# Optimization experiments

Measured on AMD Instinct MI355X. Metric: run time of the kernel, lower is better.

## Reference

```python
import jax, jax.numpy as jnp
import numpy as np

N = 20000      # nodes
E = 640000     # edges (avg degree 32)
F = 6          # feature_dim
D = 128        # weight_dim
L = 3          # lstm num_layers
DEPTH = 10     # extra iterations after initial call


def setup_inputs() -> dict:
    key = jax.random.key(0)
    ks = jax.random.split(key, 10)
    s = 0.05
    return {
        "features": jax.random.normal(ks[0], (N, F), jnp.float32),
        "src": jax.random.randint(ks[1], (E,), 0, N),
        "dst": jax.random.randint(ks[2], (E,), 0, N),
        "W_in": jax.random.normal(ks[3], (F, D), jnp.float32) * s,
        "b_in": jnp.zeros((D,), jnp.float32),
        "Wih0": jax.random.normal(ks[4], (4 * D, 2 * D), jnp.float32) * s,   # layer 0: input = concat(h_in, feat)
        "Wih_rest": jax.random.normal(ks[5], (2, 4 * D, D), jnp.float32) * s,  # layers 1,2
        "Whh": jax.random.normal(ks[6], (L, 4 * D, D), jnp.float32) * s,
        "bih": jnp.zeros((L, 4 * D), jnp.float32),
        "bhh": jnp.zeros((L, 4 * D), jnp.float32),
        "W_out": jax.random.normal(ks[7], (D, 1), jnp.float32) * s,
        "b_out": jnp.zeros((1,), jnp.float32),
    }


def _lstm_cell(x, h, c, Wih, Whh, b):
    # PyTorch gate order: i, f, g, o
    gates = x @ Wih.T + h @ Whh.T + b              # [N, 4D]
    i, f, g, o = jnp.split(gates, 4, axis=-1)
    i = jax.nn.sigmoid(i)
    f = jax.nn.sigmoid(f)
    o = jax.nn.sigmoid(o)
    g = jnp.tanh(g)
    c_new = f * c + i * g
    h_new = o * jnp.tanh(c_new)
    return h_new, c_new


def reference(features, src, dst, W_in, b_in, Wih0, Wih_rest, Whh, bih, bhh, W_out, b_out):
    n = features.shape[0]
    b = bih + bhh                                   # [L, 4D]

    def agg(x):
        # DGL update_all(copy_src, mean): mean over incoming edges (src -> dst)
        s = jax.ops.segment_sum(x[src], dst, num_segments=n)
        deg = jax.ops.segment_sum(jnp.ones((src.shape[0],), x.dtype), dst, num_segments=n)
        return jnp.where(deg[:, None] > 0, s / jnp.maximum(deg, 1.0)[:, None], 0.0)

    feat = jax.nn.relu(features @ W_in + b_in)      # [N, D]
    h = jnp.zeros((L, n, D), features.dtype)
    c = jnp.zeros((L, n, D), features.dtype)

    def step(carry, _):
        feat, h, c = carry
        x0 = jnp.concatenate([agg(feat), feat], axis=-1)   # [N, 2D]
        h0, c0 = _lstm_cell(x0, h[0], c[0], Wih0, Whh[0], b[0])
        h1, c1 = _lstm_cell(h0, h[1], c[1], Wih_rest[0], Whh[1], b[1])
        h2, c2 = _lstm_cell(h1, h[2], c[2], Wih_rest[1], Whh[2], b[2])
        return (h2, jnp.stack([h0, h1, h2]), jnp.stack([c0, c1, c2])), None

    # initial call + depth extra iterations, all structurally identical
    (feat, h, c), _ = jax.lax.scan(step, (feat, h, c), None, length=1 + DEPTH)
    return h[-1] @ W_out + b_out                    # [N, 1]
```

## Files before the change

### kernel.cpp

```cpp
#include <hip/hip_runtime.h>
#include <math.h>

typedef _Float16 f16;
typedef __attribute__((ext_vector_type(8))) _Float16 half8;
typedef __attribute__((ext_vector_type(4))) float float4v;

__device__ __forceinline__ float fast_sigmoid(float x) { return 1.0f / (1.0f + __expf(-x)); }
__device__ __forceinline__ float fast_tanh(float x) {
    float a = fabsf(x);
    float e = __expf(-2.0f * a);
    float t = (1.0f - e) / (1.0f + e);
    return copysignf(t, x);
}

__device__ __forceinline__ void async_copy16(const void* gsrc, void* ldst) {
    __builtin_amdgcn_global_load_lds(
        (const __attribute__((address_space(1))) void*)gsrc,
        (__attribute__((address_space(3))) void*)ldst,
        16, 0, 0);
}

__global__ void packb_kernel(const float* __restrict__ Wih, int Kih,
                             const float* __restrict__ Whh, int K,
                             const float* __restrict__ bih, const float* __restrict__ bhh,
                             f16* __restrict__ Bp, float* __restrict__ bp) {
    int t = blockIdx.x * blockDim.x + threadIdx.x;
    if (t >= (K << 9)) return;
    int colp = t / K;
    int k = t - colp * K;
    int dg = colp >> 6, q = (colp >> 4) & 3, dl = colp & 15;
    int j = q * 128 + dg * 16 + dl;
    float v = (k < Kih) ? Wih[j * Kih + k] : Whh[j * (K - Kih) + (k - Kih)];
    Bp[t] = (f16)v;
    if (k == 0) bp[colp] = bih[j] + bhh[j];
}

__global__ void feat0_kernel(const float* __restrict__ features, const float* __restrict__ W_in,
                             const float* __restrict__ b_in, f16* __restrict__ feat, int n) {
    int t = blockIdx.x * blockDim.x + threadIdx.x;
    if (t >= n * 128) return;
    int node = t >> 7;
    int d = t & 127;
    float s = b_in[d];
#pragma unroll
    for (int k = 0; k < 6; ++k) s += features[node * 6 + k] * W_in[k * 128 + d];
    feat[t] = (f16)fmaxf(s, 0.0f);
}

__global__ void hist_kernel(const int* __restrict__ dst, int* __restrict__ cnt, int e) {
    int t = blockIdx.x * blockDim.x + threadIdx.x;
    if (t < e) atomicAdd(&cnt[dst[t]], 1);
}

__global__ void scan_kernel(const int* __restrict__ cnt, int* __restrict__ off,
                            int* __restrict__ cur, float* __restrict__ recip, int n) {
    __shared__ int wsum[16];
    __shared__ int stot;
    int t = threadIdx.x;
    int lane = t & 63, wv = t >> 6;
    int R = 0;
    int rounds = (n + 1023) >> 10;
    for (int i = 0; i < rounds; ++i) {
        int idx = (i << 10) + t;
        int v = (idx < n) ? cnt[idx] : 0;
        int s = v;
#pragma unroll
        for (int o = 1; o < 64; o <<= 1) {
            int u = __shfl_up(s, o, 64);
            if (lane >= o) s += u;
        }
        if (lane == 63) wsum[wv] = s;
        __syncthreads();
        if (t == 0) {
            int a = 0;
#pragma unroll
            for (int j = 0; j < 16; ++j) { int x = wsum[j]; wsum[j] = a; a += x; }
            stot = a;
        }
        __syncthreads();
        int excl = R + wsum[wv] + s - v;
        if (idx < n) {
            off[idx] = excl; cur[idx] = excl;
            recip[idx] = (v > 0) ? 1.0f / (float)v : 0.0f;
        }
        R += stot;
        __syncthreads();
    }
    if (t == 0) off[n] = R;
}

__global__ void scatter_kernel(const int* __restrict__ src, const int* __restrict__ dst,
                               int* __restrict__ cur, int* __restrict__ esrc, int e) {
    int t = blockIdx.x * blockDim.x + threadIdx.x;
    if (t >= e) return;
    int d = dst[t];
    int p = atomicAdd(&cur[d], 1);
    esrc[p] = src[t];
}

__global__ __launch_bounds__(256, 6) void agg_kernel(
    const f16* __restrict__ feat, const int* __restrict__ off,
    const int* __restrict__ esrc, const float* __restrict__ recip,
    f16* __restrict__ agg, int n) {
    int slot = threadIdx.x >> 4;
    int lane = threadIdx.x & 15;
    int v = blockIdx.x * 16 + slot;
    if (v >= n) return;
    int e0 = off[v], e1 = off[v + 1];
    float a[8];
#pragma unroll
    for (int j = 0; j < 8; ++j) a[j] = 0.0f;
    int e = e0;
    for (; e + 8 <= e1; e += 8) {
        int ss[8];
#pragma unroll
        for (int u = 0; u < 8; ++u) ss[u] = esrc[e + u];
        half8 vv[8];
#pragma unroll
        for (int u = 0; u < 8; ++u)
            vv[u] = *(const half8*)&feat[(size_t)ss[u] * 128 + lane * 8];
#pragma unroll
        for (int u = 0; u < 8; ++u)
#pragma unroll
            for (int j = 0; j < 8; ++j) a[j] += (float)vv[u][j];
    }
    for (; e < e1; ++e) {
        int s = esrc[e];
        half8 v0 = *(const half8*)&feat[(size_t)s * 128 + lane * 8];
#pragma unroll
        for (int j = 0; j < 8; ++j) a[j] += (float)v0[j];
    }
    float r = recip[v];
    half8 o;
#pragma unroll
    for (int j = 0; j < 8; ++j) o[j] = (f16)(a[j] * r);
    *(half8*)&agg[(size_t)v * 128 + lane * 8] = o;
}

#define BM 64

template <int PARTS>
__global__ __launch_bounds__(256, 3) void gemm_lstm(
    const f16* __restrict__ A0, const f16* __restrict__ A1, const f16* __restrict__ A2,
    const f16* __restrict__ Bp, const float* __restrict__ bp,
    float* __restrict__ c, f16* __restrict__ h_out, int nrows) {
    constexpr int K = PARTS * 128;
    __shared__ f16 As[64 * 32];
    __shared__ f16 Bs[256 * 32];

    const int tid = threadIdx.x;
    const int w = tid >> 6;
    const int lane = tid & 63;
    const int dl = lane & 15;
    const int quad = lane >> 4;
    const int row0 = blockIdx.x * BM;
    const int cb = blockIdx.y;

    float4v acc[4][4];
#pragma unroll
    for (int q = 0; q < 4; ++q) {
        float b = bp[cb * 256 + w * 64 + q * 16 + dl];
#pragma unroll
        for (int rt = 0; rt < 4; ++rt) {
            acc[rt][q][0] = b; acc[rt][q][1] = b; acc[rt][q][2] = b; acc[rt][q][3] = b;
        }
    }

    const int srow = lane >> 2;
    const int sj = lane & 3;
    const int sg = sj ^ ((srow >> 1) & 3);
    const int rslot = (quad ^ ((dl >> 1) & 3)) << 3;

    for (int kt = 0; kt < PARTS * 4; ++kt) {
        const f16* Ap = A0;
        const int pi = kt >> 2;
        if (PARTS >= 2 && pi == 1) Ap = A1;
        if (PARTS >= 3 && pi == 2) Ap = A2;
        const int kk = (kt & 3) * 32;

        __syncthreads();
        async_copy16(&Ap[(size_t)(row0 + w * 16 + srow) * 128 + kk + (sg << 3)],
                     (f16*)As + w * 512);
        const f16* Bbase = Bp + (size_t)(cb * 256) * K + kt * 32;
#pragma unroll
        for (int i = 0; i < 4; ++i) {
            int m = i * 4 + w;
            async_copy16(&Bbase[(size_t)(m * 16 + srow) * K + (sg << 3)],
                         (f16*)Bs + m * 512);
        }
        __syncthreads();

        half8 a[4], b[4];
#pragma unroll
        for (int rt = 0; rt < 4; ++rt)
            a[rt] = *(const half8*)&As[(rt * 16 + dl) * 32 + rslot];
#pragma unroll
        for (int q = 0; q < 4; ++q)
            b[q] = *(const half8*)&Bs[((w * 4 + q) * 16 + dl) * 32 + rslot];
#pragma unroll
        for (int rt = 0; rt < 4; ++rt)
#pragma unroll
            for (int q = 0; q < 4; ++q)
                acc[rt][q] = __builtin_amdgcn_mfma_f32_16x16x32_f16(a[rt], b[q], acc[rt][q], 0, 0, 0);
    }

    const int d = cb * 64 + w * 16 + dl;
#pragma unroll
    for (int rt = 0; rt < 4; ++rt) {
#pragma unroll
        for (int r = 0; r < 4; ++r) {
            int n = row0 + rt * 16 + (quad << 2) + r;
            if (n < nrows) {
                float ig = fast_sigmoid(acc[rt][0][r]);
                float fg = fast_sigmoid(acc[rt][1][r]);
                float gg = fast_tanh(acc[rt][2][r]);
                float og = fast_sigmoid(acc[rt][3][r]);
                float cold = c[(size_t)n * 128 + d];
                float cn = fg * cold + ig * gg;
                c[(size_t)n * 128 + d] = cn;
                h_out[(size_t)n * 128 + d] = (f16)(og * fast_tanh(cn));
            }
        }
    }
}

__global__ void out_kernel(const f16* __restrict__ h2, const float* __restrict__ Wout,
                           const float* __restrict__ bout, float* __restrict__ out) {
    int n = blockIdx.x;
    int l = threadIdx.x;
    float v = (float)h2[(size_t)n * 128 + l] * Wout[l] +
              (float)h2[(size_t)n * 128 + 64 + l] * Wout[64 + l];
#pragma unroll
    for (int o = 32; o > 0; o >>= 1) v += __shfl_down(v, o, 64);
    if (l == 0) out[n] = v + bout[0];
}

extern "C" void kernel_launch(void* const* d_in, const int* in_sizes, int n_in,
                              void* d_out, int out_size, void* d_ws, size_t ws_size,
                              hipStream_t stream) {
    const float* features = (const float*)d_in[0];
    const int*   src      = (const int*)d_in[1];
    const int*   dst      = (const int*)d_in[2];
    const float* W_in     = (const float*)d_in[3];
    const float* b_in     = (const float*)d_in[4];
    const float* Wih0     = (const float*)d_in[5];
    const float* Wih_rest = (const float*)d_in[6];
    const float* Whh      = (const float*)d_in[7];
    const float* bih      = (const float*)d_in[8];
    const float* bhh      = (const float*)d_in[9];
    const float* W_out    = (const float*)d_in[10];
    const float* b_out    = (const float*)d_in[11];
    float* out = (float*)d_out;

    const int N = in_sizes[0] / 6;
    const int E = in_sizes[1];
    const int NP = N + BM;

    char* ws = (char*)d_ws;
    size_t pos = 0;
    auto alloc = [&](size_t bytes) -> void* {
        void* p = ws + pos;
        pos = (pos + bytes + 255) & ~(size_t)255;
        return p;
    };
    const size_t hrow = 128;
    const size_t hbytes = (size_t)NP * hrow * sizeof(f16);
    const size_t cbytes = (size_t)NP * hrow * sizeof(float);
    f16* feath = (f16*)alloc(hbytes);
    f16* aggh  = (f16*)alloc(hbytes);
    f16* hblk  = (f16*)alloc(6 * hbytes);
    f16* hA[3], * hB[3];
    for (int l = 0; l < 3; ++l) {
        hA[l] = hblk + (size_t)l * NP * hrow;
        hB[l] = hblk + (size_t)(l + 3) * NP * hrow;
    }
    float* cblk = (float*)alloc(3 * cbytes);
    float* c0 = cblk + 0 * (size_t)NP * hrow;
    float* c1 = cblk + 1 * (size_t)NP * hrow;
    float* c2 = cblk + 2 * (size_t)NP * hrow;
    f16* Bp0 = (f16*)alloc((size_t)512 * 384 * sizeof(f16));
    f16* Bp1 = (f16*)alloc((size_t)512 * 256 * sizeof(f16));
    f16* Bp2 = (f16*)alloc((size_t)512 * 256 * sizeof(f16));
    float* bp0 = (float*)alloc(512 * sizeof(float));
    float* bp1 = (float*)alloc(512 * sizeof(float));
    float* bp2 = (float*)alloc(512 * sizeof(float));
    int*   cnt   = (int*)alloc((size_t)N * 4);
    int*   offs  = (int*)alloc((size_t)(N + 1) * 4);
    int*   cur   = (int*)alloc((size_t)N * 4);
    int*   esrc  = (int*)alloc((size_t)E * 4);
    float* recip = (float*)alloc((size_t)N * 4);

    hipMemsetAsync(hblk, 0, 6 * hbytes, stream);
    hipMemsetAsync(cblk, 0, 3 * cbytes, stream);
    hipMemsetAsync(cnt, 0, (size_t)N * 4, stream);

    packb_kernel<<<(512 * 384 + 255) / 256, 256, 0, stream>>>(
        Wih0, 256, Whh, 384, bih, bhh, Bp0, bp0);
    packb_kernel<<<(512 * 256 + 255) / 256, 256, 0, stream>>>(
        Wih_rest, 128, Whh + 512 * 128, 256, bih + 512, bhh + 512, Bp1, bp1);
    packb_kernel<<<(512 * 256 + 255) / 256, 256, 0, stream>>>(
        Wih_rest + 512 * 128, 128, Whh + 2 * 512 * 128, 256, bih + 1024, bhh + 1024, Bp2, bp2);

    feat0_kernel<<<(N * 128 + 255) / 256, 256, 0, stream>>>(features, W_in, b_in, feath, N);
    hist_kernel<<<(E + 255) / 256, 256, 0, stream>>>(dst, cnt, E);
    scan_kernel<<<1, 1024, 0, stream>>>(cnt, offs, cur, recip, N);
    scatter_kernel<<<(E + 255) / 256, 256, 0, stream>>>(src, dst, cur, esrc, E);

    const dim3 ggrid((N + BM - 1) / BM, 2, 1);
    const int gagg = (N + 15) / 16;
    const f16* featcur = feath;
    f16 *r0 = hA[0], *r1 = hA[1], *r2 = hA[2];
    f16 *w0 = hB[0], *w1 = hB[1], *w2 = hB[2];
    for (int step = 0; step < 11; ++step) {
        agg_kernel<<<gagg, 256, 0, stream>>>(featcur, offs, esrc, recip, aggh, N);
        gemm_lstm<3><<<ggrid, 256, 0, stream>>>(aggh, featcur, r0, Bp0, bp0, c0, w0, N);
        gemm_lstm<2><<<ggrid, 256, 0, stream>>>(w0, r1, nullptr, Bp1, bp1, c1, w1, N);
        gemm_lstm<2><<<ggrid, 256, 0, stream>>>(w1, r2, nullptr, Bp2, bp2, c2, w2, N);
        featcur = w2;
        f16* t;
        t = r0; r0 = w0; w0 = t;
        t = r1; r1 = w1; w1 = t;
        t = r2; r2 = w2; w2 = t;
    }
    out_kernel<<<N, 64, 0, stream>>>((const f16*)featcur, W_out, b_out, out);
}
```

Before: 1.097 ms.

## Fuse aggregation and three LSTM layers into one per-step kernel

Replaces the per-step aggregation kernel and three GEMM+LSTM kernels with a single kernel. Each 64-row block gathers neighbor means into LDS, then runs all three layers over the full 512 gate columns, passing each layer's h output to the next through LDS. The cell state moves to a block-private tiled layout so it is read and written as float4 vectors. The aim is to cut three launches per step and the global round-trips for agg, h0 and h1. In exchange each block holds a larger accumulator (4x8 MFMA tiles), occupancy drops to 2 blocks per CU, and the grid halves with no column split.

```diff
diff --git a/kernel.cpp b/kernel.cpp
--- a/kernel.cpp
+++ b/kernel.cpp
@@ -98,130 +98,172 @@
     esrc[p] = src[t];
 }
 
-__global__ __launch_bounds__(256, 6) void agg_kernel(
-    const f16* __restrict__ feat, const int* __restrict__ off,
-    const int* __restrict__ esrc, const float* __restrict__ recip,
-    f16* __restrict__ agg, int n) {
-    int slot = threadIdx.x >> 4;
-    int lane = threadIdx.x & 15;
-    int v = blockIdx.x * 16 + slot;
-    if (v >= n) return;
-    int e0 = off[v], e1 = off[v + 1];
-    float a[8];
-#pragma unroll
-    for (int j = 0; j < 8; ++j) a[j] = 0.0f;
-    int e = e0;
-    for (; e + 8 <= e1; e += 8) {
-        int ss[8];
-#pragma unroll
-        for (int u = 0; u < 8; ++u) ss[u] = esrc[e + u];
-        half8 vv[8];
-#pragma unroll
-        for (int u = 0; u < 8; ++u)
-            vv[u] = *(const half8*)&feat[(size_t)ss[u] * 128 + lane * 8];
-#pragma unroll
-        for (int u = 0; u < 8; ++u)
-#pragma unroll
-            for (int j = 0; j < 8; ++j) a[j] += (float)vv[u][j];
-    }
-    for (; e < e1; ++e) {
-        int s = esrc[e];
-        half8 v0 = *(const half8*)&feat[(size_t)s * 128 + lane * 8];
-#pragma unroll
-        for (int j = 0; j < 8; ++j) a[j] += (float)v0[j];
-    }
-    float r = recip[v];
-    half8 o;
-#pragma unroll
-    for (int j = 0; j < 8; ++j) o[j] = (f16)(a[j] * r);
-    *(half8*)&agg[(size_t)v * 128 + lane * 8] = o;
-}
-
-#define BM 64
-
-template <int PARTS>
-__global__ __launch_bounds__(256, 3) void gemm_lstm(
-    const f16* __restrict__ A0, const f16* __restrict__ A1, const f16* __restrict__ A2,
+
+template <int NKT, bool HL>
+__device__ __forceinline__ void lstm_layer(
+    f16* aggb, f16* achk, f16* Bs,
+    const f16* __restrict__ A1, const f16* __restrict__ A2,
     const f16* __restrict__ Bp, const float* __restrict__ bp,
-    float* __restrict__ c, f16* __restrict__ h_out, int nrows) {
-    constexpr int K = PARTS * 128;
-    __shared__ f16 As[64 * 32];
-    __shared__ f16 Bs[256 * 32];
+    float* __restrict__ cl, f16* __restrict__ hg,
+    float4v (&acc)[4][8],
+    int row0, int n, int w, int dl, int quad,
+    int srow, int sg, int rslot) {
+    constexpr int KK = NKT * 32;
+
+#pragma unroll
+    for (int j = 0; j < 8; ++j) {
+        float bb = bp[(w * 8 + j) * 16 + dl];
+#pragma unroll
+        for (int rt = 0; rt < 4; ++rt) {
+            acc[rt][j][0] = bb; acc[rt][j][1] = bb; acc[rt][j][2] = bb; acc[rt][j][3] = bb;
+        }
+    }
+
+    for (int kt = 0; kt < NKT; ++kt) {
+        const int p = kt >> 2, tloc = kt & 3;
+        __syncthreads();
+#pragma unroll
+        for (int i = 0; i < 8; ++i) {
+            int m = w * 8 + i;
+            async_copy16(&Bp[(size_t)(m * 16 + srow) * KK + kt * 32 + (sg << 3)],
+                         (f16*)Bs + m * 512);
+        }
+        if (p > 0) {
+            const f16* Ag = (p == 1) ? A1 : A2;
+            async_copy16(&Ag[(size_t)(row0 + w * 16 + srow) * 128 + tloc * 32 + (sg << 3)],
+                         (f16*)achk + w * 512);
+        }
+        __syncthreads();
+
+        half8 a[4], b[8];
+        if (p == 0) {
+            const int slotA = (((tloc << 2) + quad) ^ (dl & 7)) << 3;
+#pragma unroll
+            for (int rt = 0; rt < 4; ++rt)
+                a[rt] = *(const half8*)&aggb[(rt * 16 + dl) * 128 + slotA];
+        } else {
+#pragma unroll
+            for (int rt = 0; rt < 4; ++rt)
+                a[rt] = *(const half8*)&achk[(rt * 16 + dl) * 32 + rslot];
+        }
+#pragma unroll
+        for (int j = 0; j < 8; ++j)
+            b[j] = *(const half8*)&Bs[((w * 8 + j) * 16 + dl) * 32 + rslot];
+#pragma unroll
+        for (int rt = 0; rt < 4; ++rt)
+#pragma unroll
+            for (int j = 0; j < 8; ++j)
+                acc[rt][j] = __builtin_amdgcn_mfma_f32_16x16x32_f16(a[rt], b[j], acc[rt][j], 0, 0, 0);
+    }
+
+#pragma unroll
+    for (int rt = 0; rt < 4; ++rt) {
+#pragma unroll
+        for (int dt = 0; dt < 2; ++dt) {
+            float4v ig = acc[rt][dt * 4 + 0], fg = acc[rt][dt * 4 + 1];
+            float4v gg = acc[rt][dt * 4 + 2], og = acc[rt][dt * 4 + 3];
+            float* cp = cl + ((rt * 2 + dt) << 10) + ((int)threadIdx.x << 2);
+            float4v cold = *(const float4v*)cp;
+            float4v cn;
+            float hn[4];
+#pragma unroll
+            for (int r = 0; r < 4; ++r) {
+                float i_ = fast_sigmoid(ig[r]);
+                float f_ = fast_sigmoid(fg[r]);
+                float g_ = fast_tanh(gg[r]);
+                float o_ = fast_sigmoid(og[r]);
+                float cv = f_ * cold[r] + i_ * g_;
+                cn[r] = cv;
+                hn[r] = o_ * fast_tanh(cv);
+            }
+            *(float4v*)cp = cn;
+            const int d = w * 32 + dt * 16 + dl;
+#pragma unroll
+            for (int r = 0; r < 4; ++r) {
+                int np = rt * 16 + (quad << 2) + r;
+                f16 hv = (f16)hn[r];
+                if (row0 + np < n) hg[(size_t)(row0 + np) * 128 + d] = hv;
+                if (HL)
+                    aggb[np * 128 + ((((d >> 3) ^ (np & 7))) << 3) + (d & 7)] = hv;
+            }
+        }
+    }
+}
+
+__global__ __launch_bounds__(256, 2) void fused_step(
+    const f16* __restrict__ feat,
+    const f16* __restrict__ r0, const f16* __restrict__ r1, const f16* __restrict__ r2,
+    const int* __restrict__ off, const int* __restrict__ esrc, const float* __restrict__ recip,
+    const f16* __restrict__ Bp0, const float* __restrict__ bp0,
+    const f16* __restrict__ Bp1, const float* __restrict__ bp1,
+    const f16* __restrict__ Bp2, const float* __restrict__ bp2,
+    float* __restrict__ c0, float* __restrict__ c1, float* __restrict__ c2,
+    f16* __restrict__ w0, f16* __restrict__ w1, f16* __restrict__ w2,
+    int n) {
+    __shared__ f16 aggb[64 * 128];
+    __shared__ f16 achk[64 * 32];
+    __shared__ f16 Bs[512 * 32];
 
     const int tid = threadIdx.x;
-    const int w = tid >> 6;
-    const int lane = tid & 63;
-    const int dl = lane & 15;
-    const int quad = lane >> 4;
-    const int row0 = blockIdx.x * BM;
-    const int cb = blockIdx.y;
-
-    float4v acc[4][4];
-#pragma unroll
-    for (int q = 0; q < 4; ++q) {
-        float b = bp[cb * 256 + w * 64 + q * 16 + dl];
-#pragma unroll
-        for (int rt = 0; rt < 4; ++rt) {
-            acc[rt][q][0] = b; acc[rt][q][1] = b; acc[rt][q][2] = b; acc[rt][q][3] = b;
+    const int w = tid >> 6, lane = tid & 63;
+    const int dl = lane & 15, quad = lane >> 4;
+    const int row0 = blockIdx.x * 64;
+
+    {
+        const int slot = tid >> 4, l16 = tid & 15;
+        for (int rd = 0; rd < 4; ++rd) {
+            const int np = rd * 16 + slot;
+            const int v = row0 + np;
+            float a[8];
+#pragma unroll
+            for (int j = 0; j < 8; ++j) a[j] = 0.0f;
+            if (v < n) {
+                const int e1 = off[v + 1];
+                int e = off[v];
+                for (; e + 8 <= e1; e += 8) {
+                    int ss[8];
+#pragma unroll
+                    for (int u = 0; u < 8; ++u) ss[u] = esrc[e + u];
+                    half8 vv[8];
+#pragma unroll
+                    for (int u = 0; u < 8; ++u)
+                        vv[u] = *(const half8*)&feat[(size_t)ss[u] * 128 + l16 * 8];
+#pragma unroll
+                    for (int u = 0; u < 8; ++u)
+#pragma unroll
+                        for (int j = 0; j < 8; ++j) a[j] += (float)vv[u][j];
+                }
+                for (; e < e1; ++e) {
+                    half8 v0 = *(const half8*)&feat[(size_t)esrc[e] * 128 + l16 * 8];
+#pragma unroll
+                    for (int j = 0; j < 8; ++j) a[j] += (float)v0[j];
+                }
+                const float rc = recip[v];
+#pragma unroll
+                for (int j = 0; j < 8; ++j) a[j] *= rc;
+            }
+            half8 o;
+#pragma unroll
+            for (int j = 0; j < 8; ++j) o[j] = (f16)a[j];
+            *(half8*)&aggb[np * 128 + ((l16 ^ (np & 7)) << 3)] = o;
         }
     }
 
     const int srow = lane >> 2;
-    const int sj = lane & 3;
-    const int sg = sj ^ ((srow >> 1) & 3);
+    const int sg = (lane & 3) ^ ((srow >> 1) & 3);
     const int rslot = (quad ^ ((dl >> 1) & 3)) << 3;
 
-    for (int kt = 0; kt < PARTS * 4; ++kt) {
-        const f16* Ap = A0;
-        const int pi = kt >> 2;
-        if (PARTS >= 2 && pi == 1) Ap = A1;
-        if (PARTS >= 3 && pi == 2) Ap = A2;
-        const int kk = (kt & 3) * 32;
-
-        __syncthreads();
-        async_copy16(&Ap[(size_t)(row0 + w * 16 + srow) * 128 + kk + (sg << 3)],
-                     (f16*)As + w * 512);
-        const f16* Bbase = Bp + (size_t)(cb * 256) * K + kt * 32;
-#pragma unroll
-        for (int i = 0; i < 4; ++i) {
-            int m = i * 4 + w;
-            async_copy16(&Bbase[(size_t)(m * 16 + srow) * K + (sg << 3)],
-                         (f16*)Bs + m * 512);
-        }
-        __syncthreads();
-
-        half8 a[4], b[4];
-#pragma unroll
-        for (int rt = 0; rt < 4; ++rt)
-            a[rt] = *(const half8*)&As[(rt * 16 + dl) * 32 + rslot];
-#pragma unroll
-        for (int q = 0; q < 4; ++q)
-            b[q] = *(const half8*)&Bs[((w * 4 + q) * 16 + dl) * 32 + rslot];
-#pragma unroll
-        for (int rt = 0; rt < 4; ++rt)
-#pragma unroll
-            for (int q = 0; q < 4; ++q)
-                acc[rt][q] = __builtin_amdgcn_mfma_f32_16x16x32_f16(a[rt], b[q], acc[rt][q], 0, 0, 0);
-    }
-
-    const int d = cb * 64 + w * 16 + dl;
-#pragma unroll
-    for (int rt = 0; rt < 4; ++rt) {
-#pragma unroll
-        for (int r = 0; r < 4; ++r) {
-            int n = row0 + rt * 16 + (quad << 2) + r;
-            if (n < nrows) {
-                float ig = fast_sigmoid(acc[rt][0][r]);
-                float fg = fast_sigmoid(acc[rt][1][r]);
-                float gg = fast_tanh(acc[rt][2][r]);
-                float og = fast_sigmoid(acc[rt][3][r]);
-                float cold = c[(size_t)n * 128 + d];
-                float cn = fg * cold + ig * gg;
-                c[(size_t)n * 128 + d] = cn;
-                h_out[(size_t)n * 128 + d] = (f16)(og * fast_tanh(cn));
-            }
-        }
-    }
+    float4v acc[4][8];
+    float* cb0 = c0 + (size_t)blockIdx.x * 8192;
+    float* cb1 = c1 + (size_t)blockIdx.x * 8192;
+    float* cb2 = c2 + (size_t)blockIdx.x * 8192;
+
+    lstm_layer<12, true >(aggb, achk, Bs, feat, r0, Bp0, bp0, cb0, w0, acc,
+                          row0, n, w, dl, quad, srow, sg, rslot);
+    lstm_layer< 8, true >(aggb, achk, Bs, r1, r1, Bp1, bp1, cb1, w1, acc,
+                          row0, n, w, dl, quad, srow, sg, rslot);
+    lstm_layer< 8, false>(aggb, achk, Bs, r2, r2, Bp2, bp2, cb2, w2, acc,
+                          row0, n, w, dl, quad, srow, sg, rslot);
 }
 
 __global__ void out_kernel(const f16* __restrict__ h2, const float* __restrict__ Wout,
@@ -254,7 +296,8 @@
 
     const int N = in_sizes[0] / 6;
     const int E = in_sizes[1];
-    const int NP = N + BM;
+    const int NP = N + 64;
+    const int NBLK = (N + 63) / 64;
 
     char* ws = (char*)d_ws;
     size_t pos = 0;
@@ -267,7 +310,6 @@
     const size_t hbytes = (size_t)NP * hrow * sizeof(f16);
     const size_t cbytes = (size_t)NP * hrow * sizeof(float);
     f16* feath = (f16*)alloc(hbytes);
-    f16* aggh  = (f16*)alloc(hbytes);
     f16* hblk  = (f16*)alloc(6 * hbytes);
     f16* hA[3], * hB[3];
     for (int l = 0; l < 3; ++l) {
@@ -293,6 +335,7 @@
     hipMemsetAsync(hblk, 0, 6 * hbytes, stream);
     hipMemsetAsync(cblk, 0, 3 * cbytes, stream);
     hipMemsetAsync(cnt, 0, (size_t)N * 4, stream);
+    hipMemsetAsync(feath + (size_t)N * hrow, 0, (size_t)(NP - N) * hrow * sizeof(f16), stream);
 
     packb_kernel<<<(512 * 384 + 255) / 256, 256, 0, stream>>>(
         Wih0, 256, Whh, 384, bih, bhh, Bp0, bp0);
@@ -306,16 +349,14 @@
     scan_kernel<<<1, 1024, 0, stream>>>(cnt, offs, cur, recip, N);
     scatter_kernel<<<(E + 255) / 256, 256, 0, stream>>>(src, dst, cur, esrc, E);
 
-    const dim3 ggrid((N + BM - 1) / BM, 2, 1);
-    const int gagg = (N + 15) / 16;
     const f16* featcur = feath;
     f16 *r0 = hA[0], *r1 = hA[1], *r2 = hA[2];
     f16 *w0 = hB[0], *w1 = hB[1], *w2 = hB[2];
     for (int step = 0; step < 11; ++step) {
-        agg_kernel<<<gagg, 256, 0, stream>>>(featcur, offs, esrc, recip, aggh, N);
-        gemm_lstm<3><<<ggrid, 256, 0, stream>>>(aggh, featcur, r0, Bp0, bp0, c0, w0, N);
-        gemm_lstm<2><<<ggrid, 256, 0, stream>>>(w0, r1, nullptr, Bp1, bp1, c1, w1, N);
-        gemm_lstm<2><<<ggrid, 256, 0, stream>>>(w1, r2, nullptr, Bp2, bp2, c2, w2, N);
+        fused_step<<<NBLK, 256, 0, stream>>>(
+            featcur, r0, r1, r2, offs, esrc, recip,
+            Bp0, bp0, Bp1, bp1, Bp2, bp2,
+            c0, c1, c2, w0, w1, w2, N);
         featcur = w2;
         f16* t;
         t = r0; r0 = w0; w0 = t;
```

Measured after the change: 1.565 ms. 1.43x slower.

## Double-buffer LDS tiles in LSTM GEMM and use block-private coalesced cell state

Applied to the files above, without the earlier changes.

Splits the shared-memory A/B tiles into two buffers so the async global-to-LDS load of the next K-tile is issued while MFMAs run on the current one. This cuts the barriers per K step from two to one. The LSTM cell state is moved to a block-private layout indexed by block and thread, so each thread reads and writes it as one float4 instead of scattered scalar accesses. The cost is double the LDS use, which may lower occupancy. The cell-state write no longer checks the row bound, so it relies on the c buffer covering padded rows.

```diff
diff --git a/kernel.cpp b/kernel.cpp
--- a/kernel.cpp
+++ b/kernel.cpp
@@ -145,8 +145,9 @@
     const f16* __restrict__ Bp, const float* __restrict__ bp,
     float* __restrict__ c, f16* __restrict__ h_out, int nrows) {
     constexpr int K = PARTS * 128;
-    __shared__ f16 As[64 * 32];
-    __shared__ f16 Bs[256 * 32];
+    constexpr int NT = PARTS * 4;
+    __shared__ f16 As[2][64 * 32];
+    __shared__ f16 Bs[2][256 * 32];
 
     const int tid = threadIdx.x;
     const int w = tid >> 6;
@@ -171,55 +172,70 @@
     const int sg = sj ^ ((srow >> 1) & 3);
     const int rslot = (quad ^ ((dl >> 1) & 3)) << 3;
 
-    for (int kt = 0; kt < PARTS * 4; ++kt) {
+    auto stage = [&](int kt, int bsel) {
         const f16* Ap = A0;
         const int pi = kt >> 2;
         if (PARTS >= 2 && pi == 1) Ap = A1;
         if (PARTS >= 3 && pi == 2) Ap = A2;
         const int kk = (kt & 3) * 32;
-
-        __syncthreads();
         async_copy16(&Ap[(size_t)(row0 + w * 16 + srow) * 128 + kk + (sg << 3)],
-                     (f16*)As + w * 512);
+                     (f16*)As[bsel] + w * 512);
         const f16* Bbase = Bp + (size_t)(cb * 256) * K + kt * 32;
 #pragma unroll
         for (int i = 0; i < 4; ++i) {
             int m = i * 4 + w;
             async_copy16(&Bbase[(size_t)(m * 16 + srow) * K + (sg << 3)],
-                         (f16*)Bs + m * 512);
-        }
-        __syncthreads();
+                         (f16*)Bs[bsel] + m * 512);
+        }
+    };
+
+    stage(0, 0);
+    __syncthreads();
+
+    for (int kt = 0; kt < NT; ++kt) {
+        const int cur = kt & 1;
+        if (kt + 1 < NT) stage(kt + 1, cur ^ 1);
 
         half8 a[4], b[4];
 #pragma unroll
         for (int rt = 0; rt < 4; ++rt)
-            a[rt] = *(const half8*)&As[(rt * 16 + dl) * 32 + rslot];
+            a[rt] = *(const half8*)&As[cur][(rt * 16 + dl) * 32 + rslot];
 #pragma unroll
         for (int q = 0; q < 4; ++q)
-            b[q] = *(const half8*)&Bs[((w * 4 + q) * 16 + dl) * 32 + rslot];
+            b[q] = *(const half8*)&Bs[cur][((w * 4 + q) * 16 + dl) * 32 + rslot];
 #pragma unroll
         for (int rt = 0; rt < 4; ++rt)
 #pragma unroll
             for (int q = 0; q < 4; ++q)
                 acc[rt][q] = __builtin_amdgcn_mfma_f32_16x16x32_f16(a[rt], b[q], acc[rt][q], 0, 0, 0);
-    }
-
+
+        __syncthreads();
+    }
+
+    float* cpriv = c + ((size_t)(blockIdx.x * 2 + cb)) * 4096;
     const int d = cb * 64 + w * 16 + dl;
 #pragma unroll
     for (int rt = 0; rt < 4; ++rt) {
+        float4v ig = acc[rt][0], fg = acc[rt][1], gg = acc[rt][2], og = acc[rt][3];
+        float* cp = cpriv + rt * 1024 + tid * 4;
+        float4v cold = *(const float4v*)cp;
+        float4v cn;
+        float hn[4];
 #pragma unroll
         for (int r = 0; r < 4; ++r) {
-            int n = row0 + rt * 16 + (quad << 2) + r;
-            if (n < nrows) {
-                float ig = fast_sigmoid(acc[rt][0][r]);
-                float fg = fast_sigmoid(acc[rt][1][r]);
-                float gg = fast_tanh(acc[rt][2][r]);
-                float og = fast_sigmoid(acc[rt][3][r]);
-                float cold = c[(size_t)n * 128 + d];
-                float cn = fg * cold + ig * gg;
-                c[(size_t)n * 128 + d] = cn;
-                h_out[(size_t)n * 128 + d] = (f16)(og * fast_tanh(cn));
-            }
+            float i_ = fast_sigmoid(ig[r]);
+            float f_ = fast_sigmoid(fg[r]);
+            float g_ = fast_tanh(gg[r]);
+            float o_ = fast_sigmoid(og[r]);
+            float cv = f_ * cold[r] + i_ * g_;
+            cn[r] = cv;
+            hn[r] = o_ * fast_tanh(cv);
+        }
+        *(float4v*)cp = cn;
+#pragma unroll
+        for (int r = 0; r < 4; ++r) {
+            int nr = row0 + rt * 16 + (quad << 2) + r;
+            if (nr < nrows) h_out[(size_t)nr * 128 + d] = (f16)hn[r];
         }
     }
 }
```

After: 1.080 ms. About the same (-1.5%).
